# Kernel optimization log

Measured on AMD Instinct MI355X. Metric: run time of the kernel, lower is better.

Reference implementation:

```python
import jax, jax.numpy as jnp
import numpy as np

NEG = -10000.0
EMB = 64
HID = 128


def _lstm_dir(x_tbf, Wih, Whh, b):
    # x_tbf: [T, B, EMB]; Wih: [4H, EMB]; Whh: [4H, H]; b: [4H]
    B = x_tbf.shape[1]
    h0 = jnp.zeros((B, HID), x_tbf.dtype)
    c0 = jnp.zeros((B, HID), x_tbf.dtype)

    def step(carry, xt):
        h, c = carry
        z = xt @ Wih.T + h @ Whh.T + b  # [B, 4H]
        i, f, g, o = jnp.split(z, 4, axis=-1)
        c = jax.nn.sigmoid(f) * c + jax.nn.sigmoid(i) * jnp.tanh(g)
        h = jax.nn.sigmoid(o) * jnp.tanh(c)
        return (h, c), h

    _, hs = jax.lax.scan(step, (h0, c0), x_tbf)
    return hs  # [T, B, H]


def _crf_logZ(feats, trans):
    # feats: [B, T, K]; trans[next, prev]
    B, T, K = feats.shape
    fv0 = jnp.full((B, K), NEG, feats.dtype).at[:, 0].set(0.0)

    def step(fv, emit_t):  # fv [B,K], emit_t [B,K]
        s = fv[:, None, :] + trans[None, :, :] + emit_t[:, :, None]  # [B,next,prev]
        return jax.nn.logsumexp(s, axis=2), None

    fv, _ = jax.lax.scan(step, fv0, jnp.swapaxes(feats, 0, 1))
    return jax.nn.logsumexp(fv + trans[0][None, :], axis=1)  # [B]


def _gold_score(feats, tags, trans):
    # feats: [B,T,K], tags: [B,T]
    B, T, K = feats.shape
    prev = jnp.concatenate([jnp.zeros((B, 1), tags.dtype), tags[:, :-1]], axis=1)
    trans_sc = trans[tags, prev].sum(axis=1)  # [B]
    emit_sc = jnp.take_along_axis(feats, tags[:, :, None], axis=2)[..., 0].sum(axis=1)
    stop_sc = trans[0, tags[:, -1]]
    return trans_sc + emit_sc + stop_sc


def setup_inputs() -> dict:
    key = jax.random.key(0)
    ks = jax.random.split(key, 12)
    V, K, B, T = 32000, 32, 128, 512
    sentences = jax.random.randint(ks[0], (B, T), 0, V)
    tags = jax.random.randint(ks[1], (B, T), 0, K)
    emb = jax.random.normal(ks[2], (V, EMB), jnp.float32) * 0.1
    s_ih = 1.0 / np.sqrt(HID)
    Wih_f = jax.random.uniform(ks[3], (4 * HID, EMB), jnp.float32, -s_ih, s_ih)
    Whh_f = jax.random.uniform(ks[4], (4 * HID, HID), jnp.float32, -s_ih, s_ih)
    b_f = jax.random.uniform(ks[5], (4 * HID,), jnp.float32, -s_ih, s_ih)
    Wih_b = jax.random.uniform(ks[6], (4 * HID, EMB), jnp.float32, -s_ih, s_ih)
    Whh_b = jax.random.uniform(ks[7], (4 * HID, HID), jnp.float32, -s_ih, s_ih)
    b_b = jax.random.uniform(ks[8], (4 * HID,), jnp.float32, -s_ih, s_ih)
    s_o = 1.0 / np.sqrt(2 * HID)
    W_out = jax.random.uniform(ks[9], (K, 2 * HID), jnp.float32, -s_o, s_o)
    b_out = jax.random.uniform(ks[10], (K,), jnp.float32, -s_o, s_o)
    trans = jax.random.normal(ks[11], (K, K), jnp.float32)
    trans = trans.at[:, 0].set(NEG).at[0, :].set(NEG)
    return {"sentences": sentences, "tags": tags, "emb": emb,
            "Wih_f": Wih_f, "Whh_f": Whh_f, "b_f": b_f,
            "Wih_b": Wih_b, "Whh_b": Whh_b, "b_b": b_b,
            "W_out": W_out, "b_out": b_out, "trans": trans}


def reference(sentences, tags, emb, Wih_f, Whh_f, b_f, Wih_b, Whh_b, b_b, W_out, b_out, trans):
    x = emb[sentences]                      # [B, T, EMB]
    x_tbf = jnp.swapaxes(x, 0, 1)           # [T, B, EMB]
    h_f = _lstm_dir(x_tbf, Wih_f, Whh_f, b_f)
    h_b = _lstm_dir(x_tbf[::-1], Wih_b, Whh_b, b_b)[::-1]
    h = jnp.concatenate([h_f, h_b], axis=-1)  # [T, B, 256]
    feats = jnp.swapaxes(h, 0, 1) @ W_out.T + b_out  # [B, T, K]
    logZ = _crf_logZ(feats, trans)
    gold = _gold_score(feats, tags, trans)
    return logZ.sum() - gold.sum()
```

## Files before the change

### kernel.cpp

```cpp
#include <hip/hip_runtime.h>
#include <stdint.h>

typedef short bf16x8 __attribute__((ext_vector_type(8)));
typedef float f32x4 __attribute__((ext_vector_type(4)));

#define NEG (-10000.0f)
#define LOG2E 1.44269504089f
#define LN2 0.69314718056f
#define EXP2F(x) __builtin_amdgcn_exp2f(x)
#define LOG2F(x) __builtin_amdgcn_logf(x)
#define RCPF(x) __builtin_amdgcn_rcpf(x)
constexpr int T_LEN = 512;
constexpr int BATCH = 128;

__device__ __forceinline__ unsigned short f2bf(float f) {
    union { float f; unsigned u; } v; v.f = f;
    return (unsigned short)((v.u + 0x7FFFu + ((v.u >> 16) & 1u)) >> 16);
}
__device__ __forceinline__ float bf2f(unsigned short s) {
    union { unsigned u; float f; } v; v.u = (unsigned)s << 16; return v.f;
}
__device__ __forceinline__ unsigned short f2bf_fast(float f) {
    unsigned r;
    asm("v_cvt_pk_bf16_f32 %0, %1, %2" : "=v"(r) : "v"(f), "v"(f));
    return (unsigned short)r;
}
__device__ __forceinline__ float rlanef(float x, int l) {
    union { float f; int i; } a, r;
    a.f = x;
    r.i = __builtin_amdgcn_readlane(a.i, l);
    return r.f;
}
__device__ __forceinline__ f32x4 mfma16(bf16x8 a, bf16x8 b, f32x4 c) {
    return __builtin_amdgcn_mfma_f32_16x16x32_bf16(a, b, c, 0, 0, 0);
}

__global__ void __launch_bounds__(256) k_embed(const int* __restrict__ sent,
                                               const float* __restrict__ emb,
                                               unsigned short* __restrict__ xt) {
    int gid = blockIdx.x * 256 + threadIdx.x;
    int row = gid >> 5;
    int p   = gid & 31;
    int w = sent[row];
    float2 v = *(const float2*)(emb + (size_t)w * 64 + p * 2);
    unsigned o;
    asm("v_cvt_pk_bf16_f32 %0, %1, %2" : "=v"(o) : "v"(v.x), "v"(v.y));
    ((unsigned*)xt)[(size_t)row * 32 + p] = o;
}

__global__ void __launch_bounds__(512, 2) k_lstm(
        const unsigned short* __restrict__ xt,
        const float* __restrict__ Wih_f, const float* __restrict__ Whh_f, const float* __restrict__ b_f,
        const float* __restrict__ Wih_b, const float* __restrict__ Whh_b, const float* __restrict__ b_b,
        unsigned short* __restrict__ hbuf) {
    const int tid  = threadIdx.x;
    const int lane = tid & 63;
    const int w    = tid >> 6;
    const int b    = blockIdx.x & 127;
    const int dir  = blockIdx.x >> 7;

    const float* Wih  = dir ? Wih_b : Wih_f;
    const float* Whh  = dir ? Whh_b : Whh_f;
    const float* bias = dir ? b_b   : b_f;

    __shared__ __align__(16) unsigned short zbuf[2][32][512];
    __shared__ __align__(16) unsigned short hl[2][128];

    const int nlo = lane & 15;
    const int kg  = lane >> 4;
    const int u   = 16 * w + nlo;

    bf16x8 hfrag[4][4];
    #pragma unroll
    for (int g = 0; g < 4; ++g) {
        const float sc = (g == 2) ? (-2.0f * LOG2E) : (-LOG2E);
        const int j = 128 * g + u;
        #pragma unroll
        for (int kt = 0; kt < 4; ++kt) {
            const float* src = Whh + (size_t)j * 128 + 32 * kt + kg * 8;
            bf16x8 tmp;
            #pragma unroll
            for (int q = 0; q < 8; ++q) tmp[q] = (short)f2bf(src[q] * sc);
            hfrag[g][kt] = tmp;
        }
    }
    bf16x8 wx[4][2];
    float bsc[4];
    #pragma unroll
    for (int nt = 0; nt < 4; ++nt) {
        const int n = 64 * w + 16 * nt + nlo;
        const float scn = ((n >> 7) == 2) ? (-2.0f * LOG2E) : (-LOG2E);
        bsc[nt] = bias[n] * scn;
        #pragma unroll
        for (int kt = 0; kt < 2; ++kt) {
            const float* src = Wih + (size_t)n * 64 + 32 * kt + kg * 8;
            bf16x8 tmp;
            #pragma unroll
            for (int q = 0; q < 8; ++q) tmp[q] = (short)f2bf(src[q] * scn);
            wx[nt][kt] = tmp;
        }
    }

    const unsigned short* xb = xt + (size_t)b * T_LEN * 64;

    auto load_x = [&](int c, bf16x8 xf[2][2]) {
        const int tb = dir ? (511 - 32 * c) : (32 * c);
        #pragma unroll
        for (int rt = 0; rt < 2; ++rt) {
            const int m = 16 * rt + nlo;
            const int t = dir ? (tb - m) : (tb + m);
            xf[rt][0] = *(const bf16x8*)(xb + t * 64 + kg * 8);
            xf[rt][1] = *(const bf16x8*)(xb + t * 64 + 32 + kg * 8);
        }
    };
    auto zx_phase = [&](int buf, bf16x8 xf[2][2]) {
        #pragma unroll
        for (int rt = 0; rt < 2; ++rt) {
            #pragma unroll
            for (int nt = 0; nt < 4; ++nt) {
                f32x4 a = (f32x4){bsc[nt], bsc[nt], bsc[nt], bsc[nt]};
                a = mfma16(xf[rt][0], wx[nt][0], a);
                a = mfma16(xf[rt][1], wx[nt][1], a);
                const int n = 64 * w + 16 * nt + nlo;
                const int base = (n & 127) * 4 + (n >> 7);
                #pragma unroll
                for (int r = 0; r < 4; ++r)
                    zbuf[buf][16 * rt + 4 * kg + r][base] = f2bf(a[r]);
            }
        }
    };

    if (tid < 128) { hl[0][tid] = 0; hl[1][tid] = 0; }
    bf16x8 xfA[2][2], xfB[2][2];
    load_x(0, xfA);
    zx_phase(0, xfA);
    load_x(1, xfB);
    __syncthreads();

    float c = 0.0f;
    const f32x4 z4 = (f32x4){0.f, 0.f, 0.f, 0.f};
    unsigned short* hbp = hbuf + ((size_t)b * T_LEN + (dir ? 511 : 0)) * 256 + dir * 128 + u;
    const ptrdiff_t hstep = dir ? -256 : 256;

    for (int ch = 0; ch < 16; ++ch) {
        const int p = ch & 1;
        if (ch + 1 < 16) zx_phase(1 - p, p ? xfA : xfB);
        if (ch + 2 < 16) load_x(ch + 2, p ? xfB : xfA);

        #pragma unroll 2
        for (int s = 0; s < 32; ++s) {
            const int gs = 32 * ch + s;
            const int hp = gs & 1;

            ushort4 zv = *(const ushort4*)(&zbuf[p][s][u * 4]);
            const unsigned short* hr = hl[hp];
            bf16x8 h0 = *(const bf16x8*)(hr      + kg * 8);
            bf16x8 h1 = *(const bf16x8*)(hr + 32 + kg * 8);
            bf16x8 h2 = *(const bf16x8*)(hr + 64 + kg * 8);
            bf16x8 h3 = *(const bf16x8*)(hr + 96 + kg * 8);

            f32x4 ai = mfma16(h0, hfrag[0][0], z4);
            f32x4 af = mfma16(h0, hfrag[1][0], z4);
            f32x4 ag = mfma16(h0, hfrag[2][0], z4);
            f32x4 ao = mfma16(h0, hfrag[3][0], z4);
            #pragma unroll
            for (int kt = 1; kt < 4; ++kt) {
                bf16x8 hh = (kt == 1) ? h1 : (kt == 2) ? h2 : h3;
                ai = mfma16(hh, hfrag[0][kt], ai);
                af = mfma16(hh, hfrag[1][kt], af);
                ag = mfma16(hh, hfrag[2][kt], ag);
                ao = mfma16(hh, hfrag[3][kt], ao);
            }

            float zi = bf2f(zv.x), zf = bf2f(zv.y), zg = bf2f(zv.z), zo = bf2f(zv.w);
            float ig = RCPF(1.0f + EXP2F(ai[0] + zi));
            float fg = RCPF(1.0f + EXP2F(af[0] + zf));
            float tg = 2.0f * RCPF(1.0f + EXP2F(ag[0] + zg)) - 1.0f;
            float og = RCPF(1.0f + EXP2F(ao[0] + zo));
            c = fg * c + ig * tg;
            float tc = 2.0f * RCPF(1.0f + EXP2F(-2.0f * LOG2E * c)) - 1.0f;
            unsigned short hv = f2bf_fast(og * tc);

            if (kg == 0) {
                hl[1 - hp][u] = hv;
                *hbp = hv;
            }
            hbp += hstep;
            __asm__ volatile("" ::: "memory");
            __builtin_amdgcn_s_waitcnt(0xc07f);
            __builtin_amdgcn_s_barrier();
            __asm__ volatile("" ::: "memory");
        }
    }
}

__global__ void __launch_bounds__(256) k_feats(const unsigned short* __restrict__ hbuf,
                                               const float* __restrict__ Wout,
                                               const float* __restrict__ bout,
                                               float* __restrict__ feats) {
    const int lane = threadIdx.x & 63;
    const int wv   = blockIdx.x * 4 + (threadIdx.x >> 6);
    const int nlo  = lane & 15, kg = lane >> 4;

    bf16x8 bw[2][8];
    #pragma unroll
    for (int nt = 0; nt < 2; ++nt) {
        const float* src0 = Wout + (size_t)(nt * 16 + nlo) * 256 + kg * 8;
        #pragma unroll
        for (int kt = 0; kt < 8; ++kt) {
            bf16x8 tmp;
            #pragma unroll
            for (int q = 0; q < 8; ++q) tmp[q] = (short)f2bf(src0[kt * 32 + q]);
            bw[nt][kt] = tmp;
        }
    }
    float bb0 = bout[nlo], bb1 = bout[16 + nlo];

    for (int rg = 0; rg < 4; ++rg) {
        int row0 = wv * 64 + rg * 16;
        f32x4 a0 = {0.f,0.f,0.f,0.f}, a1 = {0.f,0.f,0.f,0.f};
        #pragma unroll
        for (int kt = 0; kt < 8; ++kt) {
            bf16x8 a = *(const bf16x8*)(hbuf + (size_t)(row0 + nlo) * 256 + kt * 32 + kg * 8);
            a0 = mfma16(a, bw[0][kt], a0);
            a1 = mfma16(a, bw[1][kt], a1);
        }
        #pragma unroll
        for (int r = 0; r < 4; ++r) {
            size_t rr = (size_t)(row0 + kg * 4 + r) * 32;
            feats[rr + nlo]      = a0[r] + bb0;
            feats[rr + 16 + nlo] = a1[r] + bb1;
        }
    }
}

__global__ void __launch_bounds__(64) k_crf(const float* __restrict__ feats,
                                            const float* __restrict__ trans,
                                            const int* __restrict__ tags,
                                            float* __restrict__ out) {
    const int b    = blockIdx.x;
    const int lane = threadIdx.x;
    const int k1   = lane & 31;

    __shared__ float str[1024];
    for (int i = lane; i < 1024; i += 64) str[i] = trans[i];

    float E[32];
    float sumE = 0.0f;
    #pragma unroll
    for (int j = 0; j < 32; ++j) {
        E[j] = EXP2F(trans[k1 * 32 + j] * LOG2E);
        sumE += E[j];
    }
    __syncthreads();

    const int* tg = tags + (size_t)b * T_LEN;
    const float* fb = feats + (size_t)b * T_LEN * 32;
    float gsum = 0.0f;
    for (int t = lane; t < T_LEN; t += 64) {
        int cur = tg[t];
        int prev = t ? tg[t - 1] : 0;
        gsum += str[cur * 32 + prev] + fb[(size_t)t * 32 + cur];
    }
    #pragma unroll
    for (int o = 32; o >= 1; o >>= 1) gsum += __shfl_xor(gsum, o);

    float coff = NEG * LOG2E;
    float fv2  = coff + LOG2F(1.0f + sumE) + fb[k1] * LOG2E;
    coff = rlanef(fv2, 16);
    float evA = fb[32 + k1] * LOG2E;
    float evB = fb[64 + k1] * LOG2E;

    for (int t = 1; t < T_LEN; ++t) {
        float evC = (t + 2 < T_LEN) ? fb[(size_t)(t + 2) * 32 + k1] : 0.0f;
        float u = EXP2F(fv2 - coff);
        float p0 = 0.f, p1 = 0.f, p2 = 0.f, p3 = 0.f;
        #pragma unroll
        for (int j = 0; j < 32; j += 4) {
            p0 += E[j]     * rlanef(u, j);
            p1 += E[j + 1] * rlanef(u, j + 1);
            p2 += E[j + 2] * rlanef(u, j + 2);
            p3 += E[j + 3] * rlanef(u, j + 3);
        }
        float p = (p0 + p1) + (p2 + p3);
        p = fmaxf(p, 1e-37f);
        fv2  = coff + LOG2F(p) + evA;
        coff = rlanef(fv2, 16);
        evA = evB; evB = evC * LOG2E;
    }

    float v2 = fv2 + str[k1] * LOG2E;
    float m2 = v2;
    #pragma unroll
    for (int o = 32; o >= 1; o >>= 1) m2 = fmaxf(m2, __shfl_xor(m2, o));
    float e = EXP2F(v2 - m2);
    #pragma unroll
    for (int o = 32; o >= 1; o >>= 1) e += __shfl_xor(e, o);
    float logZ = LN2 * (m2 + LOG2F(e) - 1.0f);

    if (lane == 0) {
        float gold = gsum + str[tg[T_LEN - 1]];
        atomicAdd(out, logZ - gold);
    }
}

extern "C" void kernel_launch(void* const* d_in, const int* in_sizes, int n_in,
                              void* d_out, int out_size, void* d_ws, size_t ws_size,
                              hipStream_t stream) {
    const int*   sent  = (const int*)d_in[0];
    const int*   tags  = (const int*)d_in[1];
    const float* emb   = (const float*)d_in[2];
    const float* Wih_f = (const float*)d_in[3];
    const float* Whh_f = (const float*)d_in[4];
    const float* b_f   = (const float*)d_in[5];
    const float* Wih_b = (const float*)d_in[6];
    const float* Whh_b = (const float*)d_in[7];
    const float* b_b   = (const float*)d_in[8];
    const float* Wout  = (const float*)d_in[9];
    const float* bout  = (const float*)d_in[10];
    const float* trans = (const float*)d_in[11];
    (void)in_sizes; (void)n_in; (void)ws_size;

    char* ws = (char*)d_ws;
    unsigned short* hbuf  = (unsigned short*)ws;
    float*          feats = (float*)(ws + 33554432);
    unsigned short* xt    = (unsigned short*)(ws + 33554432 + 8388608);

    (void)hipMemsetAsync(d_out, 0, sizeof(float) * out_size, stream);
    k_embed<<<8192, 256, 0, stream>>>(sent, emb, xt);
    k_lstm <<<256,  512, 0, stream>>>(xt, Wih_f, Whh_f, b_f, Wih_b, Whh_b, b_b, hbuf);
    k_feats<<<256,  256, 0, stream>>>(hbuf, Wout, bout, feats);
    k_crf  <<<BATCH, 64, 0, stream>>>(feats, trans, tags, (float*)d_out);
}
```

Baseline: 440.0 us.

## Fuse output projection into CRF kernel, keeping per-batch feats in LDS

Merges the feats projection kernel into the CRF kernel. Each 256-thread block computes the 512x32 emission scores for its batch row with MFMA and writes them into padded shared memory, so they never round-trip through global memory. One wave then runs the forward recursion while another computes the gold score. This removes a kernel launch and the global feats write and read. The cost is a 66KB LDS footprint per block and fewer blocks (128 instead of 256) doing the projection.

Result: no change. 434.8 us (-1.2%).

```diff
diff --git a/kernel.cpp b/kernel.cpp
--- a/kernel.cpp
+++ b/kernel.cpp
@@ -149,8 +149,7 @@
 
         #pragma unroll 2
         for (int s = 0; s < 32; ++s) {
-            const int gs = 32 * ch + s;
-            const int hp = gs & 1;
+            const int hp = (32 * ch + s) & 1;
 
             ushort4 zv = *(const ushort4*)(&zbuf[p][s][u * 4]);
             const unsigned short* hr = hl[hp];
@@ -194,114 +193,120 @@
     }
 }
 
-__global__ void __launch_bounds__(256) k_feats(const unsigned short* __restrict__ hbuf,
-                                               const float* __restrict__ Wout,
-                                               const float* __restrict__ bout,
-                                               float* __restrict__ feats) {
-    const int lane = threadIdx.x & 63;
-    const int wv   = blockIdx.x * 4 + (threadIdx.x >> 6);
+__global__ void __launch_bounds__(256) k_crf_fused(
+        const unsigned short* __restrict__ hbuf,
+        const float* __restrict__ Wout,
+        const float* __restrict__ bout,
+        const float* __restrict__ trans,
+        const int* __restrict__ tags,
+        float* __restrict__ out) {
+    const int b    = blockIdx.x;
+    const int tid  = threadIdx.x;
+    const int lane = tid & 63;
+    const int wv   = tid >> 6;
     const int nlo  = lane & 15, kg = lane >> 4;
 
-    bf16x8 bw[2][8];
-    #pragma unroll
-    for (int nt = 0; nt < 2; ++nt) {
-        const float* src0 = Wout + (size_t)(nt * 16 + nlo) * 256 + kg * 8;
-        #pragma unroll
-        for (int kt = 0; kt < 8; ++kt) {
-            bf16x8 tmp;
-            #pragma unroll
-            for (int q = 0; q < 8; ++q) tmp[q] = (short)f2bf(src0[kt * 32 + q]);
-            bw[nt][kt] = tmp;
-        }
-    }
-    float bb0 = bout[nlo], bb1 = bout[16 + nlo];
-
-    for (int rg = 0; rg < 4; ++rg) {
-        int row0 = wv * 64 + rg * 16;
-        f32x4 a0 = {0.f,0.f,0.f,0.f}, a1 = {0.f,0.f,0.f,0.f};
-        #pragma unroll
-        for (int kt = 0; kt < 8; ++kt) {
-            bf16x8 a = *(const bf16x8*)(hbuf + (size_t)(row0 + nlo) * 256 + kt * 32 + kg * 8);
-            a0 = mfma16(a, bw[0][kt], a0);
-            a1 = mfma16(a, bw[1][kt], a1);
-        }
-        #pragma unroll
-        for (int r = 0; r < 4; ++r) {
-            size_t rr = (size_t)(row0 + kg * 4 + r) * 32;
-            feats[rr + nlo]      = a0[r] + bb0;
-            feats[rr + 16 + nlo] = a1[r] + bb1;
-        }
-    }
-}
-
-__global__ void __launch_bounds__(64) k_crf(const float* __restrict__ feats,
-                                            const float* __restrict__ trans,
-                                            const int* __restrict__ tags,
-                                            float* __restrict__ out) {
-    const int b    = blockIdx.x;
-    const int lane = threadIdx.x;
-    const int k1   = lane & 31;
-
+    __shared__ float fbl[T_LEN * 33];
     __shared__ float str[1024];
-    for (int i = lane; i < 1024; i += 64) str[i] = trans[i];
-
-    float E[32];
-    float sumE = 0.0f;
-    #pragma unroll
-    for (int j = 0; j < 32; ++j) {
-        E[j] = EXP2F(trans[k1 * 32 + j] * LOG2E);
-        sumE += E[j];
+    __shared__ float gslot;
+
+    for (int i = tid; i < 1024; i += 256) str[i] = trans[i];
+
+    {
+        bf16x8 bw[2][8];
+        #pragma unroll
+        for (int nt = 0; nt < 2; ++nt) {
+            const float* src0 = Wout + (size_t)(nt * 16 + nlo) * 256 + kg * 8;
+            #pragma unroll
+            for (int kt = 0; kt < 8; ++kt) {
+                bf16x8 tmp;
+                #pragma unroll
+                for (int q = 0; q < 8; ++q) tmp[q] = (short)f2bf(src0[kt * 32 + q]);
+                bw[nt][kt] = tmp;
+            }
+        }
+        float bb0 = bout[nlo], bb1 = bout[16 + nlo];
+        const unsigned short* hbb = hbuf + (size_t)b * T_LEN * 256;
+
+        for (int rg = 0; rg < 8; ++rg) {
+            int lr0 = wv * 128 + rg * 16;
+            f32x4 a0 = {0.f,0.f,0.f,0.f}, a1 = {0.f,0.f,0.f,0.f};
+            #pragma unroll
+            for (int kt = 0; kt < 8; ++kt) {
+                bf16x8 a = *(const bf16x8*)(hbb + (size_t)(lr0 + nlo) * 256 + kt * 32 + kg * 8);
+                a0 = mfma16(a, bw[0][kt], a0);
+                a1 = mfma16(a, bw[1][kt], a1);
+            }
+            #pragma unroll
+            for (int r = 0; r < 4; ++r) {
+                int lr = lr0 + kg * 4 + r;
+                fbl[lr * 33 + nlo]      = a0[r] + bb0;
+                fbl[lr * 33 + 16 + nlo] = a1[r] + bb1;
+            }
+        }
     }
     __syncthreads();
 
     const int* tg = tags + (size_t)b * T_LEN;
-    const float* fb = feats + (size_t)b * T_LEN * 32;
-    float gsum = 0.0f;
-    for (int t = lane; t < T_LEN; t += 64) {
-        int cur = tg[t];
-        int prev = t ? tg[t - 1] : 0;
-        gsum += str[cur * 32 + prev] + fb[(size_t)t * 32 + cur];
-    }
-    #pragma unroll
-    for (int o = 32; o >= 1; o >>= 1) gsum += __shfl_xor(gsum, o);
-
-    float coff = NEG * LOG2E;
-    float fv2  = coff + LOG2F(1.0f + sumE) + fb[k1] * LOG2E;
-    coff = rlanef(fv2, 16);
-    float evA = fb[32 + k1] * LOG2E;
-    float evB = fb[64 + k1] * LOG2E;
-
-    for (int t = 1; t < T_LEN; ++t) {
-        float evC = (t + 2 < T_LEN) ? fb[(size_t)(t + 2) * 32 + k1] : 0.0f;
-        float u = EXP2F(fv2 - coff);
-        float p0 = 0.f, p1 = 0.f, p2 = 0.f, p3 = 0.f;
-        #pragma unroll
-        for (int j = 0; j < 32; j += 4) {
-            p0 += E[j]     * rlanef(u, j);
-            p1 += E[j + 1] * rlanef(u, j + 1);
-            p2 += E[j + 2] * rlanef(u, j + 2);
-            p3 += E[j + 3] * rlanef(u, j + 3);
-        }
-        float p = (p0 + p1) + (p2 + p3);
-        p = fmaxf(p, 1e-37f);
-        fv2  = coff + LOG2F(p) + evA;
+    if (wv == 1) {
+        float gsum = 0.0f;
+        for (int t = lane; t < T_LEN; t += 64) {
+            int cur = tg[t];
+            int prev = t ? tg[t - 1] : 0;
+            gsum += str[cur * 32 + prev] + fbl[t * 33 + cur];
+        }
+        #pragma unroll
+        for (int o = 32; o >= 1; o >>= 1) gsum += __shfl_xor(gsum, o);
+        if (lane == 0) gslot = gsum + str[tg[T_LEN - 1]];
+    }
+
+    float logZ = 0.0f;
+    if (wv == 0) {
+        const int k1 = lane & 31;
+        float E[32];
+        float sumE = 0.0f;
+        #pragma unroll
+        for (int j = 0; j < 32; ++j) {
+            E[j] = EXP2F(str[k1 * 32 + j] * LOG2E);
+            sumE += E[j];
+        }
+
+        float coff = NEG * LOG2E;
+        float fv2  = coff + LOG2F(1.0f + sumE) + fbl[k1] * LOG2E;
         coff = rlanef(fv2, 16);
-        evA = evB; evB = evC * LOG2E;
-    }
-
-    float v2 = fv2 + str[k1] * LOG2E;
-    float m2 = v2;
-    #pragma unroll
-    for (int o = 32; o >= 1; o >>= 1) m2 = fmaxf(m2, __shfl_xor(m2, o));
-    float e = EXP2F(v2 - m2);
-    #pragma unroll
-    for (int o = 32; o >= 1; o >>= 1) e += __shfl_xor(e, o);
-    float logZ = LN2 * (m2 + LOG2F(e) - 1.0f);
-
-    if (lane == 0) {
-        float gold = gsum + str[tg[T_LEN - 1]];
-        atomicAdd(out, logZ - gold);
-    }
+        float evA = fbl[33 + k1] * LOG2E;
+        float evB = fbl[66 + k1] * LOG2E;
+
+        for (int t = 1; t < T_LEN; ++t) {
+            float evC = (t + 2 < T_LEN) ? fbl[(t + 2) * 33 + k1] : 0.0f;
+            float u = EXP2F(fv2 - coff);
+            float p0 = 0.f, p1 = 0.f, p2 = 0.f, p3 = 0.f;
+            #pragma unroll
+            for (int j = 0; j < 32; j += 4) {
+                p0 += E[j]     * rlanef(u, j);
+                p1 += E[j + 1] * rlanef(u, j + 1);
+                p2 += E[j + 2] * rlanef(u, j + 2);
+                p3 += E[j + 3] * rlanef(u, j + 3);
+            }
+            float p = (p0 + p1) + (p2 + p3);
+            p = fmaxf(p, 1e-37f);
+            fv2  = coff + LOG2F(p) + evA;
+            coff = rlanef(fv2, 16);
+            evA = evB; evB = evC * LOG2E;
+        }
+
+        float v2 = fv2 + str[k1] * LOG2E;
+        float m2 = v2;
+        #pragma unroll
+        for (int o = 32; o >= 1; o >>= 1) m2 = fmaxf(m2, __shfl_xor(m2, o));
+        float e = EXP2F(v2 - m2);
+        #pragma unroll
+        for (int o = 32; o >= 1; o >>= 1) e += __shfl_xor(e, o);
+        logZ = LN2 * (m2 + LOG2F(e) - 1.0f);
+    }
+
+    __syncthreads();
+    if (tid == 0) atomicAdd(out, logZ - gslot);
 }
 
 extern "C" void kernel_launch(void* const* d_in, const int* in_sizes, int n_in,
@@ -322,13 +327,11 @@
     (void)in_sizes; (void)n_in; (void)ws_size;
 
     char* ws = (char*)d_ws;
-    unsigned short* hbuf  = (unsigned short*)ws;
-    float*          feats = (float*)(ws + 33554432);
-    unsigned short* xt    = (unsigned short*)(ws + 33554432 + 8388608);
+    unsigned short* hbuf = (unsigned short*)ws;
+    unsigned short* xt   = (unsigned short*)(ws + 33554432);
 
     (void)hipMemsetAsync(d_out, 0, sizeof(float) * out_size, stream);
-    k_embed<<<8192, 256, 0, stream>>>(sent, emb, xt);
-    k_lstm <<<256,  512, 0, stream>>>(xt, Wih_f, Whh_f, b_f, Wih_b, Whh_b, b_b, hbuf);
-    k_feats<<<256,  256, 0, stream>>>(hbuf, Wout, bout, feats);
-    k_crf  <<<BATCH, 64, 0, stream>>>(feats, trans, tags, (float*)d_out);
-}
+    k_embed    <<<8192, 256, 0, stream>>>(sent, emb, xt);
+    k_lstm     <<<256,  512, 0, stream>>>(xt, Wih_f, Whh_f, b_f, Wih_b, Whh_b, b_b, hbuf);
+    k_crf_fused<<<BATCH, 256, 0, stream>>>(hbuf, Wout, bout, trans, tags, (float*)d_out);
+}
```

## Interleave two CRF batch chains per wavefront and prefetch emissions in blocks of eight

Applied to the files above, without the earlier changes.

The CRF forward kernel now processes two sequences per 64-lane block, interleaving their independent recurrences so that cross-lane reads and exp/log latency of one chain can overlap with the other. Emission values are prefetched eight timesteps ahead into registers instead of three. The grid is halved to 64 blocks, which reduces parallelism across CUs and raises register pressure, in exchange for more instruction-level parallelism on the latency-bound serial scan.

Result: slower. 488.8 us (+11.1%).

```diff
diff --git a/kernel.cpp b/kernel.cpp
--- a/kernel.cpp
+++ b/kernel.cpp
@@ -149,8 +149,7 @@
 
         #pragma unroll 2
         for (int s = 0; s < 32; ++s) {
-            const int gs = 32 * ch + s;
-            const int hp = gs & 1;
+            const int hp = (32 * ch + s) & 1;
 
             ushort4 zv = *(const ushort4*)(&zbuf[p][s][u * 4]);
             const unsigned short* hr = hl[hp];
@@ -238,7 +237,8 @@
                                             const float* __restrict__ trans,
                                             const int* __restrict__ tags,
                                             float* __restrict__ out) {
-    const int b    = blockIdx.x;
+    const int bA   = blockIdx.x;
+    const int bB   = blockIdx.x + 64;
     const int lane = threadIdx.x;
     const int k1   = lane & 31;
 
@@ -254,53 +254,89 @@
     }
     __syncthreads();
 
-    const int* tg = tags + (size_t)b * T_LEN;
-    const float* fb = feats + (size_t)b * T_LEN * 32;
-    float gsum = 0.0f;
+    const int* tgA = tags + (size_t)bA * T_LEN;
+    const int* tgB = tags + (size_t)bB * T_LEN;
+    const float* fbA = feats + (size_t)bA * T_LEN * 32;
+    const float* fbB = feats + (size_t)bB * T_LEN * 32;
+    float gsA = 0.0f, gsB = 0.0f;
     for (int t = lane; t < T_LEN; t += 64) {
-        int cur = tg[t];
-        int prev = t ? tg[t - 1] : 0;
-        gsum += str[cur * 32 + prev] + fb[(size_t)t * 32 + cur];
-    }
-    #pragma unroll
-    for (int o = 32; o >= 1; o >>= 1) gsum += __shfl_xor(gsum, o);
-
-    float coff = NEG * LOG2E;
-    float fv2  = coff + LOG2F(1.0f + sumE) + fb[k1] * LOG2E;
-    coff = rlanef(fv2, 16);
-    float evA = fb[32 + k1] * LOG2E;
-    float evB = fb[64 + k1] * LOG2E;
-
-    for (int t = 1; t < T_LEN; ++t) {
-        float evC = (t + 2 < T_LEN) ? fb[(size_t)(t + 2) * 32 + k1] : 0.0f;
-        float u = EXP2F(fv2 - coff);
-        float p0 = 0.f, p1 = 0.f, p2 = 0.f, p3 = 0.f;
-        #pragma unroll
-        for (int j = 0; j < 32; j += 4) {
-            p0 += E[j]     * rlanef(u, j);
-            p1 += E[j + 1] * rlanef(u, j + 1);
-            p2 += E[j + 2] * rlanef(u, j + 2);
-            p3 += E[j + 3] * rlanef(u, j + 3);
-        }
-        float p = (p0 + p1) + (p2 + p3);
-        p = fmaxf(p, 1e-37f);
-        fv2  = coff + LOG2F(p) + evA;
-        coff = rlanef(fv2, 16);
-        evA = evB; evB = evC * LOG2E;
-    }
-
-    float v2 = fv2 + str[k1] * LOG2E;
-    float m2 = v2;
-    #pragma unroll
-    for (int o = 32; o >= 1; o >>= 1) m2 = fmaxf(m2, __shfl_xor(m2, o));
-    float e = EXP2F(v2 - m2);
-    #pragma unroll
-    for (int o = 32; o >= 1; o >>= 1) e += __shfl_xor(e, o);
-    float logZ = LN2 * (m2 + LOG2F(e) - 1.0f);
+        int curA = tgA[t], prevA = t ? tgA[t - 1] : 0;
+        int curB = tgB[t], prevB = t ? tgB[t - 1] : 0;
+        gsA += str[curA * 32 + prevA] + fbA[(size_t)t * 32 + curA];
+        gsB += str[curB * 32 + prevB] + fbB[(size_t)t * 32 + curB];
+    }
+    #pragma unroll
+    for (int o = 32; o >= 1; o >>= 1) { gsA += __shfl_xor(gsA, o); gsB += __shfl_xor(gsB, o); }
+
+    float coffA = NEG * LOG2E, coffB = NEG * LOG2E;
+    float lz0 = LOG2F(1.0f + sumE);
+    float fvA = coffA + lz0 + fbA[k1] * LOG2E;
+    float fvB = coffB + lz0 + fbB[k1] * LOG2E;
+    coffA = rlanef(fvA, 16);
+    coffB = rlanef(fvB, 16);
+
+    float LA[8], LB[8];
+    #pragma unroll
+    for (int i = 0; i < 8; ++i) {
+        LA[i] = fbA[(size_t)(1 + i) * 32 + k1];
+        LB[i] = fbB[(size_t)(1 + i) * 32 + k1];
+    }
+
+    for (int t0 = 1; t0 < T_LEN; t0 += 8) {
+        float NA[8], NB[8];
+        #pragma unroll
+        for (int i = 0; i < 8; ++i) {
+            const int tn = t0 + 8 + i;
+            NA[i] = (tn < T_LEN) ? fbA[(size_t)tn * 32 + k1] : 0.0f;
+            NB[i] = (tn < T_LEN) ? fbB[(size_t)tn * 32 + k1] : 0.0f;
+        }
+        #pragma unroll
+        for (int i = 0; i < 8; ++i) {
+            if (t0 + i < T_LEN) {
+                float uA = EXP2F(fvA - coffA);
+                float uB = EXP2F(fvB - coffB);
+                float a0 = 0.f, a1 = 0.f, a2 = 0.f, a3 = 0.f;
+                float b0 = 0.f, b1 = 0.f, b2 = 0.f, b3 = 0.f;
+                #pragma unroll
+                for (int j = 0; j < 32; j += 4) {
+                    a0 += E[j]     * rlanef(uA, j);
+                    b0 += E[j]     * rlanef(uB, j);
+                    a1 += E[j + 1] * rlanef(uA, j + 1);
+                    b1 += E[j + 1] * rlanef(uB, j + 1);
+                    a2 += E[j + 2] * rlanef(uA, j + 2);
+                    b2 += E[j + 2] * rlanef(uB, j + 2);
+                    a3 += E[j + 3] * rlanef(uA, j + 3);
+                    b3 += E[j + 3] * rlanef(uB, j + 3);
+                }
+                float pA = (a0 + a1) + (a2 + a3);
+                float pB = (b0 + b1) + (b2 + b3);
+                pA = fmaxf(pA, 1e-37f);
+                pB = fmaxf(pB, 1e-37f);
+                fvA = coffA + LOG2F(pA) + LA[i] * LOG2E;
+                fvB = coffB + LOG2F(pB) + LB[i] * LOG2E;
+                coffA = rlanef(fvA, 16);
+                coffB = rlanef(fvB, 16);
+            }
+        }
+        #pragma unroll
+        for (int i = 0; i < 8; ++i) { LA[i] = NA[i]; LB[i] = NB[i]; }
+    }
+
+    float vA = fvA + str[k1] * LOG2E;
+    float vB = fvB + str[k1] * LOG2E;
+    float mA = vA, mB = vB;
+    #pragma unroll
+    for (int o = 32; o >= 1; o >>= 1) { mA = fmaxf(mA, __shfl_xor(mA, o)); mB = fmaxf(mB, __shfl_xor(mB, o)); }
+    float eA = EXP2F(vA - mA), eB = EXP2F(vB - mB);
+    #pragma unroll
+    for (int o = 32; o >= 1; o >>= 1) { eA += __shfl_xor(eA, o); eB += __shfl_xor(eB, o); }
+    float logZA = LN2 * (mA + LOG2F(eA) - 1.0f);
+    float logZB = LN2 * (mB + LOG2F(eB) - 1.0f);
 
     if (lane == 0) {
-        float gold = gsum + str[tg[T_LEN - 1]];
-        atomicAdd(out, logZ - gold);
+        float goldA = gsA + str[tgA[T_LEN - 1]];
+        float goldB = gsB + str[tgB[T_LEN - 1]];
+        atomicAdd(out, (logZA - goldA) + (logZB - goldB));
     }
 }
 
@@ -330,5 +366,5 @@
     k_embed<<<8192, 256, 0, stream>>>(sent, emb, xt);
     k_lstm <<<256,  512, 0, stream>>>(xt, Wih_f, Whh_f, b_f, Wih_b, Whh_b, b_b, hbuf);
     k_feats<<<256,  256, 0, stream>>>(hbuf, Wout, bout, feats);
-    k_crf  <<<BATCH, 64, 0, stream>>>(feats, trans, tags, (float*)d_out);
-}
+    k_crf  <<<64,    64, 0, stream>>>(feats, trans, tags, (float*)d_out);
+}
```
